# Kernel optimization log

Measured on AMD Instinct MI355X. Metric: run time of the kernel, lower is better.

Reference implementation:

```python
import jax, jax.numpy as jnp
import numpy as np

N, F, D, K, B, L, E, H = 12288, 128, 128, 3, 64, 256, 393216, 8
DT = 2 * D  # token dim
ALPHA = 0.5


def _mlp(h, w1, b1, w2, b2):
    return jax.nn.relu(h @ w1 + b1) @ w2 + b2


def setup_inputs() -> dict:
    key = jax.random.key(0)
    ks = jax.random.split(key, 24)
    s = 0.05
    x = jax.random.normal(ks[0], (N, F), jnp.float32)
    proj_w = jax.random.normal(ks[1], (F, D), jnp.float32) * s
    proj_b = jnp.zeros((D,), jnp.float32)
    adj_rows = jax.random.randint(ks[2], (E,), 0, N, jnp.int32)
    adj_cols = jax.random.randint(ks[3], (E,), 0, N, jnp.int32)
    adj_vals = jax.random.uniform(ks[4], (E,), jnp.float32) / 32.0
    ppr = jax.random.uniform(ks[5], (N, N), jnp.float32) * 0.01
    drnl = jax.random.uniform(ks[6], (B, N), jnp.float32) * 10.0
    src = jax.random.randint(ks[7], (B,), 0, N, jnp.int32)
    dst = jax.random.randint(ks[8], (B,), 0, N, jnp.int32)
    sample_idx = jnp.repeat(jnp.arange(B, dtype=jnp.int32), L)
    node_idx = jax.random.randint(ks[9], (B, L), 0, N, jnp.int32)
    node_idx = node_idx.at[:, 0].set(src).at[:, 1].set(dst).reshape(-1)
    enc_w1 = jax.random.normal(ks[10], (4, 2, D), jnp.float32) * 0.2
    enc_b1 = jnp.zeros((4, D), jnp.float32)
    enc_w2 = jax.random.normal(ks[11], (4, D, D), jnp.float32) * s
    enc_b2 = jnp.zeros((4, D), jnp.float32)
    struct_w1 = jax.random.normal(ks[12], (4 * D, D), jnp.float32) * s
    struct_b1 = jnp.zeros((D,), jnp.float32)
    struct_w2 = jax.random.normal(ks[13], (D, D), jnp.float32) * s
    struct_b2 = jnp.zeros((D,), jnp.float32)
    cls_tok = jax.random.normal(ks[14], (DT,), jnp.float32) * s
    wq = jax.random.normal(ks[15], (DT, DT), jnp.float32) * s
    wk = jax.random.normal(ks[16], (DT, DT), jnp.float32) * s
    wv = jax.random.normal(ks[17], (DT, DT), jnp.float32) * s
    wo = jax.random.normal(ks[18], (DT, DT), jnp.float32) * s
    return dict(x=x, proj_w=proj_w, proj_b=proj_b, adj_vals=adj_vals,
                adj_rows=adj_rows, adj_cols=adj_cols, ppr=ppr, drnl=drnl,
                src=src, dst=dst, sample_idx=sample_idx, node_idx=node_idx,
                enc_w1=enc_w1, enc_b1=enc_b1, enc_w2=enc_w2, enc_b2=enc_b2,
                struct_w1=struct_w1, struct_b1=struct_b1, struct_w2=struct_w2,
                struct_b2=struct_b2, cls_tok=cls_tok, wq=wq, wk=wk, wv=wv, wo=wo)


def reference(x, proj_w, proj_b, adj_vals, adj_rows, adj_cols, ppr, drnl,
              src, dst, sample_idx, node_idx,
              enc_w1, enc_b1, enc_w2, enc_b2,
              struct_w1, struct_b1, struct_w2, struct_b2,
              cls_tok, wq, wk, wv, wo):
    # --- re_features: feature_proj + K sparse matmul hops, APPNP-style mix ---
    feats = x @ proj_w + proj_b                      # [N, D]
    h = feats
    for _ in range(K):
        h = jax.ops.segment_sum(adj_vals[:, None] * h[adj_cols], adj_rows,
                                num_segments=N)      # sparse adj @ h
    re_x = h * (1.0 - ALPHA) + feats * ALPHA         # [N, D]

    # --- cal_heuristic: dense ppr row gather + drnl lookup ---
    n = sample_idx.shape[0]
    ppr_a = ppr[src[sample_idx], node_idx]           # [n]
    ppr_b = ppr[dst[sample_idx], node_idx]
    drnl_v = drnl[sample_idx, node_idx]
    heur = jnp.zeros((n, 4, 2), jnp.float32)
    heur = heur.at[:, 2, 0].set(ppr_a).at[:, 2, 1].set(ppr_b)
    heur = heur.at[:, 3, 0].set(drnl_v).at[:, 3, 1].set(drnl_v)

    # --- tokenizer: 4 heuristic MLPs -> structure MLP, concat node feats ---
    enc = jax.vmap(_mlp)(heur.transpose(1, 0, 2), enc_w1, enc_b1, enc_w2, enc_b2)
    struct_in = enc.transpose(1, 0, 2).reshape(n, 4 * D)   # [n, 4D] (CN,AA,PPR,DRNL)
    struct = _mlp(struct_in, struct_w1, struct_b1, struct_w2, struct_b2)  # [n, D]
    tok = jnp.concatenate([struct, re_x[node_idx]], axis=-1).reshape(B, L, DT)

    # --- GraphTransformer: CLS + multi-head self-attention ---
    cls = jnp.broadcast_to(cls_tok, (B, 1, DT))
    seq = jnp.concatenate([cls, tok], axis=1)        # [B, L+1, DT]
    dh = DT // H
    q = (seq @ wq).reshape(B, L + 1, H, dh)
    k = (seq @ wk).reshape(B, L + 1, H, dh)
    v = (seq @ wv).reshape(B, L + 1, H, dh)
    att = jax.nn.softmax(jnp.einsum('bqhd,bkhd->bhqk', q, k) / jnp.sqrt(jnp.float32(dh)), axis=-1)
    out = jnp.einsum('bhqk,bkhd->bqhd', att, v).reshape(B, L + 1, DT) @ wo
    h_cls, h_a, h_b = out[:, 0], out[:, 1], out[:, 2]
    return jnp.concatenate([h_a, h_b, h_cls], axis=-1)  # [B, 6*dim]
```

## Files before the change

### kernel.cpp

```cpp
#include <hip/hip_runtime.h>
#include <math.h>

#define NN 12288
#define FD 128
#define DD 128
#define EE 393216
#define BB 64
#define LL 256
#define HH 8
#define DTD 256
#define NTOK 16384
#define NSEQ 16448
#define CAP 128

#define SC_B0   0
#define PROJ_B0 1536
#define PREP_B0 1728
#define HEUR_B0 2880
#define SBIAS_B 2944
#define SETUP_GRID 2945

typedef float f32x4 __attribute__((ext_vector_type(4)));
typedef short s16x8 __attribute__((ext_vector_type(8)));

__device__ __forceinline__ float relu_(float x){ return fmaxf(x, 0.0f); }

__device__ __forceinline__ unsigned short f2b(float f){
  unsigned int u = __float_as_uint(f);
  u += 0x7FFFu + ((u >> 16) & 1u);
  return (unsigned short)(u >> 16);
}
__device__ __forceinline__ float b2f(unsigned short h){
  return __uint_as_float(((unsigned int)h) << 16);
}

__device__ __forceinline__ f32x4 MF(s16x8 a, s16x8 b, f32x4 c){
  return __builtin_amdgcn_mfma_f32_16x16x32_bf16(a, b, c, 0, 0, 0);
}

__global__ void __launch_bounds__(256)
k_setup(const float* __restrict__ x, const float* __restrict__ proj_w,
        const float* __restrict__ proj_b, unsigned short* __restrict__ featsb,
        const float* __restrict__ wq, const float* __restrict__ wk,
        const float* __restrict__ wv,
        const float* __restrict__ enc_w2, const float* __restrict__ sw1,
        const float* __restrict__ sw2, const float* __restrict__ cls_tok,
        unsigned short* __restrict__ wqT, unsigned short* __restrict__ wkT,
        unsigned short* __restrict__ wvT,
        unsigned short* __restrict__ w2T2, unsigned short* __restrict__ w2T3,
        unsigned short* __restrict__ sw1aT, unsigned short* __restrict__ sw1bT,
        unsigned short* __restrict__ sw2T, unsigned short* __restrict__ seqb,
        const int* __restrict__ node_idx, const int* __restrict__ srcI,
        const int* __restrict__ dstI, const float* __restrict__ ppr,
        const float* __restrict__ drnl, float* __restrict__ heurA,
        float* __restrict__ heurB, float* __restrict__ heurD,
        const int* __restrict__ adj_rows, const int* __restrict__ adj_cols,
        const float* __restrict__ adj_vals, int* __restrict__ cnt,
        uint2* __restrict__ ccv,
        const float* __restrict__ enc_b1, const float* __restrict__ enc_b2,
        const float* __restrict__ sb1, float* __restrict__ sbias){
  int t = threadIdx.x;
  if(blockIdx.x < PROJ_B0){
    int e = blockIdx.x*256 + t;
    int r = adj_rows[e];
    int p = atomicAdd(&cnt[r], 1);
    ccv[(size_t)r*CAP + p] = make_uint2((unsigned)adj_cols[e], __float_as_uint(adj_vals[e]));
  } else if(blockIdx.x < PREP_B0){
    int bid = blockIdx.x - PROJ_B0;
    int row0 = bid * 64;
    int lane = t & 63, w = t >> 6;
    int lr = lane & 15, lg = lane >> 4;
    f32x4 acc[4][2];
    #pragma unroll
    for(int nt=0;nt<2;++nt){
      int col = w*32 + nt*16 + lr;
      float bv = proj_b[col];
      #pragma unroll
      for(int rt=0;rt<4;++rt)
        #pragma unroll
        for(int i=0;i<4;++i) acc[rt][nt][i]=bv;
    }
    #pragma unroll
    for(int ks=0; ks<4; ++ks){
      int kb = ks*32 + lg*8;
      s16x8 Bf[2];
      #pragma unroll
      for(int nt=0;nt<2;++nt){
        int col = w*32 + nt*16 + lr;
        #pragma unroll
        for(int i=0;i<8;++i) Bf[nt][i] = (short)f2b(proj_w[(kb+i)*DD + col]);
      }
      #pragma unroll
      for(int rt=0;rt<4;++rt){
        int row = row0 + rt*16 + lr;
        const f32x4* xp = (const f32x4*)(x + (size_t)row*FD + kb);
        f32x4 v0 = xp[0], v1 = xp[1];
        s16x8 Af;
        #pragma unroll
        for(int i=0;i<4;++i){ Af[i] = (short)f2b(v0[i]); Af[4+i] = (short)f2b(v1[i]); }
        #pragma unroll
        for(int nt=0;nt<2;++nt) acc[rt][nt] = MF(Af, Bf[nt], acc[rt][nt]);
      }
    }
    #pragma unroll
    for(int rt=0;rt<4;++rt)
      #pragma unroll
      for(int nt=0;nt<2;++nt)
        #pragma unroll
        for(int i=0;i<4;++i){
          int row = row0 + rt*16 + lg*4 + i;
          int col = w*32 + nt*16 + lr;
          featsb[(size_t)row*DD + col] = f2b(acc[rt][nt][i]);
        }
  } else if(blockIdx.x < HEUR_B0){
    int id = (blockIdx.x - PREP_B0)*256 + t;
    if(id < 196608){
      int m = id >> 16, e = id & 65535;
      int n = e & 255, k = e >> 8;
      const float* s = (m==0)? wq : (m==1)? wk : wv;
      unsigned short* d = (m==0)? wqT : (m==1)? wkT : wvT;
      d[n*256 + k] = f2b(s[k*256 + n]);
    } else if(id < 278528){
      int id2 = id - 196608;
      int m = id2 >> 14, e = id2 & 16383;
      int n = e & 127, k = e >> 7;
      const float* s;
      unsigned short* d;
      if(m==0){ s = enc_w2 + 2*16384; d = w2T2; }
      else if(m==1){ s = enc_w2 + 3*16384; d = w2T3; }
      else if(m==2){ s = sw1 + 256*128; d = sw1aT; }
      else if(m==3){ s = sw1 + 384*128; d = sw1bT; }
      else { s = sw2; d = sw2T; }
      d[n*128 + k] = f2b(s[k*128 + n]);
    } else {
      int id3 = id - 278528;
      int b = id3 >> 8, tt = id3 & 255;
      seqb[(size_t)(b*257)*DTD + tt] = f2b(cls_tok[tt]);
    }
  } else if(blockIdx.x < SBIAS_B){
    int tt = (blockIdx.x - HEUR_B0)*256 + t;
    int s = tt >> 8;
    int node = node_idx[tt];
    heurA[tt] = ppr[(size_t)srcI[s]*NN + node];
    heurB[tt] = ppr[(size_t)dstI[s]*NN + node];
    heurD[tt] = drnl[(size_t)s*NN + node];
  } else {
    __shared__ float h0[DD], h1[DD], e0[DD], e1[DD];
    if(t < DD){
      h0[t] = relu_(enc_b1[0*DD+t]);
      h1[t] = relu_(enc_b1[1*DD+t]);
    }
    __syncthreads();
    if(t < DD){
      float a0 = enc_b2[0*DD+t], a1 = enc_b2[1*DD+t];
      for(int d=0; d<DD; ++d){
        a0 += h0[d]*enc_w2[(0*DD+d)*DD + t];
        a1 += h1[d]*enc_w2[(1*DD+d)*DD + t];
      }
      e0[t]=a0; e1[t]=a1;
    }
    __syncthreads();
    if(t < DD){
      float sv = sb1[t];
      for(int d=0; d<DD; ++d)
        sv += e0[d]*sw1[d*DD + t] + e1[d]*sw1[(DD+d)*DD + t];
      sbias[t]=sv;
    }
  }
}

__global__ void __launch_bounds__(256)
k_spmm_w(const unsigned int* __restrict__ hin32, unsigned int* __restrict__ hout32,
         const int* __restrict__ cnt, const uint2* __restrict__ ccv,
         const unsigned int* __restrict__ featsb32, int finalpass){
  int lane = threadIdx.x & 63;
  int r = blockIdx.x*4 + (threadIdx.x>>6);
  int deg = cnt[r];
  const uint2* base = ccv + (size_t)r*CAP;
  float a0=0.f,a1=0.f,b0=0.f,b1=0.f,c0=0.f,c1=0.f,d0=0.f,d1=0.f;
  int p = 0;
  for(; p+4 <= deg; p += 4){
    uint2 q0 = base[p], q1 = base[p+1], q2 = base[p+2], q3 = base[p+3];
    unsigned u0 = hin32[(size_t)q0.x*64 + lane];
    unsigned u1 = hin32[(size_t)q1.x*64 + lane];
    unsigned u2 = hin32[(size_t)q2.x*64 + lane];
    unsigned u3 = hin32[(size_t)q3.x*64 + lane];
    float v0=__uint_as_float(q0.y), v1=__uint_as_float(q1.y);
    float v2=__uint_as_float(q2.y), v3=__uint_as_float(q3.y);
    a0 += v0*b2f((unsigned short)(u0&0xffffu)); a1 += v0*b2f((unsigned short)(u0>>16));
    b0 += v1*b2f((unsigned short)(u1&0xffffu)); b1 += v1*b2f((unsigned short)(u1>>16));
    c0 += v2*b2f((unsigned short)(u2&0xffffu)); c1 += v2*b2f((unsigned short)(u2>>16));
    d0 += v3*b2f((unsigned short)(u3&0xffffu)); d1 += v3*b2f((unsigned short)(u3>>16));
  }
  for(; p < deg; ++p){
    uint2 q0 = base[p];
    unsigned u0 = hin32[(size_t)q0.x*64 + lane];
    float v0 = __uint_as_float(q0.y);
    a0 += v0*b2f((unsigned short)(u0&0xffffu)); a1 += v0*b2f((unsigned short)(u0>>16));
  }
  a0 += b0 + c0 + d0;
  a1 += b1 + c1 + d1;
  if(finalpass){
    unsigned f = featsb32[(size_t)r*64 + lane];
    a0 = 0.5f*a0 + 0.5f*b2f((unsigned short)(f & 0xffffu));
    a1 = 0.5f*a1 + 0.5f*b2f((unsigned short)(f >> 16));
  }
  hout32[(size_t)r*64 + lane] = (unsigned)f2b(a0) | ((unsigned)f2b(a1) << 16);
}

__global__ void __launch_bounds__(256)
k_tok_mfma(const int* __restrict__ node_idx,
           const float* __restrict__ heurA, const float* __restrict__ heurB,
           const float* __restrict__ heurD,
           const float* __restrict__ enc_w1, const float* __restrict__ enc_b1,
           const unsigned short* __restrict__ w2T2, const unsigned short* __restrict__ w2T3,
           const float* __restrict__ enc_b2,
           const unsigned short* __restrict__ sw1aT, const unsigned short* __restrict__ sw1bT,
           const float* __restrict__ sbias,
           const unsigned short* __restrict__ sw2T, const float* __restrict__ sb2,
           const unsigned short* __restrict__ rexb, unsigned short* __restrict__ seqb){
  __shared__ float sA[64], sB[64], sDV[64];
  __shared__ int sNode[64];
  __shared__ __align__(16) unsigned short e2[64][136];
  __shared__ __align__(16) unsigned short e3[64][136];
  __shared__ __align__(16) unsigned short hid[64][136];

  int tid = threadIdx.x;
  int lane = tid & 63;
  int w = tid >> 6;
  int lr = lane & 15;
  int lg = lane >> 4;
  int t0 = blockIdx.x * 64;
  int bs = t0 >> 8;
  int p0 = t0 & 255;
  int seqrow0 = bs*257 + 1 + p0;

  if(tid < 64){
    int tt = t0 + tid;
    sNode[tid] = node_idx[tt];
    sA[tid]  = heurA[tt];
    sB[tid]  = heurB[tt];
    sDV[tid] = heurD[tt];
  }
  __syncthreads();

  {
    f32x4 acc2[4][2], acc3[4][2];
    #pragma unroll
    for(int nt=0;nt<2;++nt){
      int col = w*32 + nt*16 + lr;
      float b2v = enc_b2[2*DD + col];
      float b3v = enc_b2[3*DD + col];
      #pragma unroll
      for(int rt=0;rt<4;++rt)
        #pragma unroll
        for(int i=0;i<4;++i){ acc2[rt][nt][i]=b2v; acc3[rt][nt][i]=b3v; }
    }
    #pragma unroll
    for(int ks=0; ks<4; ++ks){
      int kb = ks*32 + lg*8;
      float w20[8], w21[8], w3s[8], b2c[8], b3c[8];
      #pragma unroll
      for(int i=0;i<8;++i){
        int k = kb + i;
        w20[i] = enc_w1[4*DD + k];
        w21[i] = enc_w1[5*DD + k];
        w3s[i] = enc_w1[6*DD + k] + enc_w1[7*DD + k];
        b2c[i] = enc_b1[2*DD + k];
        b3c[i] = enc_b1[3*DD + k];
      }
      s16x8 B2[2], B3[2];
      #pragma unroll
      for(int nt=0;nt<2;++nt){
        int col = w*32 + nt*16 + lr;
        B2[nt] = *(const s16x8*)(w2T2 + col*DD + kb);
        B3[nt] = *(const s16x8*)(w2T3 + col*DD + kb);
      }
      #pragma unroll
      for(int rt=0;rt<4;++rt){
        int row = rt*16 + lr;
        float a = sA[row], b = sB[row], dv = sDV[row];
        s16x8 A2, A3;
        #pragma unroll
        for(int i=0;i<8;++i){
          A2[i] = (short)f2b(relu_(a*w20[i] + b*w21[i] + b2c[i]));
          A3[i] = (short)f2b(relu_(dv*w3s[i] + b3c[i]));
        }
        #pragma unroll
        for(int nt=0;nt<2;++nt){
          acc2[rt][nt] = MF(A2, B2[nt], acc2[rt][nt]);
          acc3[rt][nt] = MF(A3, B3[nt], acc3[rt][nt]);
        }
      }
    }
    #pragma unroll
    for(int rt=0;rt<4;++rt)
      #pragma unroll
      for(int nt=0;nt<2;++nt)
        #pragma unroll
        for(int i=0;i<4;++i){
          int row = rt*16 + lg*4 + i;
          int col = w*32 + nt*16 + lr;
          e2[row][col] = f2b(acc2[rt][nt][i]);
          e3[row][col] = f2b(acc3[rt][nt][i]);
        }
  }
  __syncthreads();

  {
    f32x4 acc[4][2];
    #pragma unroll
    for(int nt=0;nt<2;++nt){
      int col = w*32 + nt*16 + lr;
      float sv = sbias[col];
      #pragma unroll
      for(int rt=0;rt<4;++rt)
        #pragma unroll
        for(int i=0;i<4;++i) acc[rt][nt][i]=sv;
    }
    #pragma unroll
    for(int ks=0; ks<4; ++ks){
      int kb = ks*32 + lg*8;
      s16x8 Ba[2], Bb[2];
      #pragma unroll
      for(int nt=0;nt<2;++nt){
        int col = w*32 + nt*16 + lr;
        Ba[nt] = *(const s16x8*)(sw1aT + col*DD + kb);
        Bb[nt] = *(const s16x8*)(sw1bT + col*DD + kb);
      }
      #pragma unroll
      for(int rt=0;rt<4;++rt){
        s16x8 A2 = *(const s16x8*)&e2[rt*16+lr][kb];
        s16x8 A3 = *(const s16x8*)&e3[rt*16+lr][kb];
        #pragma unroll
        for(int nt=0;nt<2;++nt){
          acc[rt][nt] = MF(A2, Ba[nt], acc[rt][nt]);
          acc[rt][nt] = MF(A3, Bb[nt], acc[rt][nt]);
        }
      }
    }
    __syncthreads();
    #pragma unroll
    for(int rt=0;rt<4;++rt)
      #pragma unroll
      for(int nt=0;nt<2;++nt)
        #pragma unroll
        for(int i=0;i<4;++i){
          int row = rt*16 + lg*4 + i;
          int col = w*32 + nt*16 + lr;
          hid[row][col] = f2b(relu_(acc[rt][nt][i]));
        }
  }
  __syncthreads();

  {
    f32x4 acc[4][2];
    #pragma unroll
    for(int nt=0;nt<2;++nt){
      int col = w*32 + nt*16 + lr;
      float bv = sb2[col];
      #pragma unroll
      for(int rt=0;rt<4;++rt)
        #pragma unroll
        for(int i=0;i<4;++i) acc[rt][nt][i]=bv;
    }
    #pragma unroll
    for(int ks=0; ks<4; ++ks){
      int kb = ks*32 + lg*8;
      s16x8 Bc[2];
      #pragma unroll
      for(int nt=0;nt<2;++nt){
        int col = w*32 + nt*16 + lr;
        Bc[nt] = *(const s16x8*)(sw2T + col*DD + kb);
      }
      #pragma unroll
      for(int rt=0;rt<4;++rt){
        s16x8 A = *(const s16x8*)&hid[rt*16+lr][kb];
        #pragma unroll
        for(int nt=0;nt<2;++nt) acc[rt][nt] = MF(A, Bc[nt], acc[rt][nt]);
      }
    }
    #pragma unroll
    for(int rt=0;rt<4;++rt)
      #pragma unroll
      for(int nt=0;nt<2;++nt)
        #pragma unroll
        for(int i=0;i<4;++i){
          int row = rt*16 + lg*4 + i;
          int col = w*32 + nt*16 + lr;
          seqb[(size_t)(seqrow0 + row)*DTD + col] = f2b(acc[rt][nt][i]);
        }
  }

  {
    int row = tid >> 2, l4 = tid & 3;
    int c = l4 * 32;
    int node = sNode[row];
    const unsigned short* rp = rexb + (size_t)node*DD + c;
    unsigned short* op = seqb + (size_t)(seqrow0 + row)*DTD + DD + c;
    #pragma unroll
    for(int j=0;j<4;++j)
      *(s16x8*)(op + j*8) = *(const s16x8*)(rp + j*8);
  }
}

__global__ void __launch_bounds__(256)
k_kv_mfma(const unsigned short* __restrict__ seqb,
          const unsigned short* __restrict__ wkT, const unsigned short* __restrict__ wvT,
          const unsigned short* __restrict__ wqT,
          unsigned short* __restrict__ kbuf, unsigned short* __restrict__ vbuf,
          float* __restrict__ qbuf){
  __shared__ __align__(16) unsigned short stile[64][276];
  int tid = threadIdx.x;
  int lane = tid & 63;
  int w = tid >> 6;
  int lr = lane & 15;
  int lg = lane >> 4;

  if(blockIdx.x < 257){
    int row0 = blockIdx.x * 64;
    int col0 = w * 64;
    f32x4 accK[4][4], accV[4][4];
    #pragma unroll
    for(int rt=0;rt<4;++rt)
      #pragma unroll
      for(int nt=0;nt<4;++nt)
        #pragma unroll
        for(int i=0;i<4;++i){ accK[rt][nt][i]=0.f; accV[rt][nt][i]=0.f; }

    #pragma unroll
    for(int ks=0; ks<8; ++ks){
      int kb = ks*32 + lg*8;
      s16x8 A[4], Bk[4], Bv[4];
      #pragma unroll
      for(int rt=0;rt<4;++rt)
        A[rt] = *(const s16x8*)(seqb + (size_t)(row0 + rt*16 + lr)*DTD + kb);
      #pragma unroll
      for(int nt=0;nt<4;++nt){
        int col = col0 + nt*16 + lr;
        Bk[nt] = *(const s16x8*)(wkT + (size_t)col*DTD + kb);
        Bv[nt] = *(const s16x8*)(wvT + (size_t)col*DTD + kb);
      }
      #pragma unroll
      for(int rt=0;rt<4;++rt)
        #pragma unroll
        for(int nt=0;nt<4;++nt){
          accK[rt][nt] = MF(A[rt], Bk[nt], accK[rt][nt]);
          accV[rt][nt] = MF(A[rt], Bv[nt], accV[rt][nt]);
        }
    }

    #pragma unroll
    for(int rt=0;rt<4;++rt)
      #pragma unroll
      for(int nt=0;nt<4;++nt)
        #pragma unroll
        for(int i=0;i<4;++i)
          stile[rt*16 + lg*4 + i][col0 + nt*16 + lr] = f2b(accK[rt][nt][i]);
    __syncthreads();
    {
      int row = tid >> 2, c = (tid & 3)*64;
      #pragma unroll
      for(int j=0;j<8;++j)
        *(s16x8*)(kbuf + (size_t)(row0+row)*DTD + c + j*8) = *(const s16x8*)&stile[row][c + j*8];
    }
    __syncthreads();
    #pragma unroll
    for(int rt=0;rt<4;++rt)
      #pragma unroll
      for(int nt=0;nt<4;++nt)
        #pragma unroll
        for(int i=0;i<4;++i)
          stile[rt*16 + lg*4 + i][col0 + nt*16 + lr] = f2b(accV[rt][nt][i]);
    __syncthreads();
    {
      int row = tid >> 2, c = (tid & 3)*64;
      #pragma unroll
      for(int j=0;j<8;++j)
        *(s16x8*)(vbuf + (size_t)(row0+row)*DTD + c + j*8) = *(const s16x8*)&stile[row][c + j*8];
    }
  } else {
    int qrow0 = (blockIdx.x - 257) * 64;
    int col0 = w * 64;
    int srow[4];
    #pragma unroll
    for(int rt=0;rt<4;++rt){
      int qr = qrow0 + rt*16 + lr;
      int bb = (qr * 21846) >> 16;
      int pp = qr - bb*3;
      srow[rt] = bb*257 + pp;
    }
    f32x4 acc[4][4];
    #pragma unroll
    for(int rt=0;rt<4;++rt)
      #pragma unroll
      for(int nt=0;nt<4;++nt)
        #pragma unroll
        for(int i=0;i<4;++i) acc[rt][nt][i]=0.f;
    #pragma unroll
    for(int ks=0; ks<8; ++ks){
      int kb = ks*32 + lg*8;
      s16x8 A[4], Bq[4];
      #pragma unroll
      for(int rt=0;rt<4;++rt)
        A[rt] = *(const s16x8*)(seqb + (size_t)srow[rt]*DTD + kb);
      #pragma unroll
      for(int nt=0;nt<4;++nt){
        int col = col0 + nt*16 + lr;
        Bq[nt] = *(const s16x8*)(wqT + (size_t)col*DTD + kb);
      }
      #pragma unroll
      for(int rt=0;rt<4;++rt)
        #pragma unroll
        for(int nt=0;nt<4;++nt)
          acc[rt][nt] = MF(A[rt], Bq[nt], acc[rt][nt]);
    }
    #pragma unroll
    for(int rt=0;rt<4;++rt)
      #pragma unroll
      for(int nt=0;nt<4;++nt)
        #pragma unroll
        for(int i=0;i<4;++i){
          int qr = qrow0 + rt*16 + lg*4 + i;
          int col = col0 + nt*16 + lr;
          qbuf[(size_t)qr*DTD + col] = acc[rt][nt][i];
        }
  }
}

__global__ void __launch_bounds__(256)
k_att2(const float* __restrict__ qbuf,
       const unsigned short* __restrict__ kbuf, const unsigned short* __restrict__ vbuf,
       float* __restrict__ att_o){
  __shared__ float q_s[3][32];
  __shared__ float sc[3][257];
  __shared__ float ppv[8][3][32];
  int t = threadIdx.x;
  int b = blockIdx.x >> 3, h = blockIdx.x & 7;

  if(t < 96){
    int qi = t>>5, dd = t&31;
    q_s[qi][dd] = qbuf[(size_t)(b*3+qi)*DTD + h*32 + dd];
  }
  __syncthreads();
  const float scale = 0.17677669529663687f;
  for(int kk=t; kk<257; kk+=256){
    const unsigned short* kr = kbuf + (size_t)(b*257+kk)*DTD + h*32;
    float kv[32];
    #pragma unroll
    for(int j=0;j<4;++j){
      s16x8 u = *(const s16x8*)(kr + j*8);
      #pragma unroll
      for(int m2=0;m2<8;++m2) kv[j*8+m2] = b2f((unsigned short)u[m2]);
    }
    float d0=0.f,d1=0.f,d2=0.f;
    #pragma unroll
    for(int dd=0;dd<32;++dd){
      d0 += q_s[0][dd]*kv[dd]; d1 += q_s[1][dd]*kv[dd]; d2 += q_s[2][dd]*kv[dd];
    }
    sc[0][kk]=d0*scale; sc[1][kk]=d1*scale; sc[2][kk]=d2*scale;
  }
  __syncthreads();
  {
    int wv = t>>6, lane = t&63;
    if(wv < 3){
      int qi = wv;
      float x0=sc[qi][lane], x1=sc[qi][lane+64], x2=sc[qi][lane+128], x3=sc[qi][lane+192];
      float x4 = (lane==0)? sc[qi][256] : -1e30f;
      float m = fmaxf(fmaxf(fmaxf(x0,x1),fmaxf(x2,x3)),x4);
      #pragma unroll
      for(int off=32; off>0; off>>=1) m = fmaxf(m, __shfl_xor(m, off));
      float e0=expf(x0-m), e1=expf(x1-m), e2v=expf(x2-m), e3v=expf(x3-m);
      float e4=(lane==0)? expf(x4-m) : 0.f;
      float s = e0+e1+e2v+e3v+e4;
      #pragma unroll
      for(int off=32; off>0; off>>=1) s += __shfl_xor(s, off);
      float inv = 1.0f/s;
      sc[qi][lane]=e0*inv; sc[qi][lane+64]=e1*inv;
      sc[qi][lane+128]=e2v*inv; sc[qi][lane+192]=e3v*inv;
      if(lane==0) sc[qi][256]=e4*inv;
    }
  }
  __syncthreads();
  {
    int dd = t & 31, g = t >> 5;
    float a0=0.f, a1=0.f, a2=0.f;
    for(int kk=g; kk<257; kk+=8){
      float v = b2f(vbuf[(size_t)(b*257+kk)*DTD + h*32 + dd]);
      a0 += sc[0][kk]*v; a1 += sc[1][kk]*v; a2 += sc[2][kk]*v;
    }
    ppv[g][0][dd]=a0; ppv[g][1][dd]=a1; ppv[g][2][dd]=a2;
  }
  __syncthreads();
  if(t < 96){
    int qi = t>>5, dd = t&31;
    float s = 0.f;
    #pragma unroll
    for(int gg=0; gg<8; ++gg) s += ppv[gg][qi][dd];
    att_o[(size_t)(b*3+qi)*DTD + h*32 + dd] = s;
  }
}

__global__ void k_out(const float* __restrict__ att_o, const float* __restrict__ wo,
                      float* __restrict__ out){
  __shared__ float srow[DTD];
  int t = threadIdx.x;
  int r = blockIdx.x;
  int b = r/3, qi = r - b*3;
  srow[t] = att_o[(size_t)r*DTD + t];
  __syncthreads();
  float acc = 0.f;
  for(int d=0; d<DTD; ++d) acc += srow[d]*wo[d*DTD + t];
  int off = (qi==1)? 0 : ((qi==2)? DTD : 2*DTD);
  out[(size_t)b*768 + off + t] = acc;
}

extern "C" void kernel_launch(void* const* d_in, const int* in_sizes, int n_in,
                              void* d_out, int out_size, void* d_ws, size_t ws_size,
                              hipStream_t stream){
  const float* x        = (const float*)d_in[0];
  const float* proj_w   = (const float*)d_in[1];
  const float* proj_b   = (const float*)d_in[2];
  const float* adj_vals = (const float*)d_in[3];
  const int*   adj_rows = (const int*)d_in[4];
  const int*   adj_cols = (const int*)d_in[5];
  const float* ppr      = (const float*)d_in[6];
  const float* drnl     = (const float*)d_in[7];
  const int*   srcI     = (const int*)d_in[8];
  const int*   dstI     = (const int*)d_in[9];
  const int*   node_idx   = (const int*)d_in[11];
  const float* enc_w1   = (const float*)d_in[12];
  const float* enc_b1   = (const float*)d_in[13];
  const float* enc_w2   = (const float*)d_in[14];
  const float* enc_b2   = (const float*)d_in[15];
  const float* sw1      = (const float*)d_in[16];
  const float* sb1      = (const float*)d_in[17];
  const float* sw2      = (const float*)d_in[18];
  const float* sb2      = (const float*)d_in[19];
  const float* cls_tok  = (const float*)d_in[20];
  const float* wq       = (const float*)d_in[21];
  const float* wk       = (const float*)d_in[22];
  const float* wv       = (const float*)d_in[23];
  const float* wo       = (const float*)d_in[24];
  float* out = (float*)d_out;

  char* p = (char*)d_ws;
  auto alloc = [&](size_t bytes)->void*{ void* r = (void*)p; p += (bytes + 63) & ~(size_t)63; return r; };
  unsigned short* featsb = (unsigned short*)alloc((size_t)NN*DD*2);
  unsigned short* h1b    = (unsigned short*)alloc((size_t)NN*DD*2);
  unsigned short* h2b    = (unsigned short*)alloc((size_t)NN*DD*2);
  unsigned short* rexb   = (unsigned short*)alloc((size_t)NN*DD*2);
  int*   cnt     = (int*)  alloc((size_t)NN*4);
  uint2* ccv     = (uint2*)alloc((size_t)NN*CAP*8);
  float* sbias   = (float*)alloc((size_t)DD*4);
  float* heurA   = (float*)alloc((size_t)NTOK*4);
  float* heurB   = (float*)alloc((size_t)NTOK*4);
  float* heurD   = (float*)alloc((size_t)NTOK*4);
  unsigned short* kbuf = (unsigned short*)alloc((size_t)NSEQ*DTD*2);
  unsigned short* vbuf = (unsigned short*)alloc((size_t)NSEQ*DTD*2);
  float* qbuf    = (float*)alloc((size_t)BB*3*DTD*4);
  float* att_o   = (float*)alloc((size_t)BB*3*DTD*4);
  unsigned short* seqb  = (unsigned short*)alloc((size_t)NSEQ*DTD*2);
  unsigned short* wqT   = (unsigned short*)alloc((size_t)DTD*DTD*2);
  unsigned short* wkT   = (unsigned short*)alloc((size_t)DTD*DTD*2);
  unsigned short* wvT   = (unsigned short*)alloc((size_t)DTD*DTD*2);
  unsigned short* w2T2  = (unsigned short*)alloc((size_t)DD*DD*2);
  unsigned short* w2T3  = (unsigned short*)alloc((size_t)DD*DD*2);
  unsigned short* sw1aT = (unsigned short*)alloc((size_t)DD*DD*2);
  unsigned short* sw1bT = (unsigned short*)alloc((size_t)DD*DD*2);
  unsigned short* sw2T  = (unsigned short*)alloc((size_t)DD*DD*2);

  hipMemsetAsync(cnt, 0, NN*sizeof(int), stream);

  k_setup   <<<SETUP_GRID, 256, 0, stream>>>(x, proj_w, proj_b, featsb,
                                             wq, wk, wv, enc_w2, sw1, sw2, cls_tok,
                                             wqT, wkT, wvT, w2T2, w2T3, sw1aT, sw1bT, sw2T, seqb,
                                             node_idx, srcI, dstI, ppr, drnl,
                                             heurA, heurB, heurD,
                                             adj_rows, adj_cols, adj_vals, cnt, ccv,
                                             enc_b1, enc_b2, sb1, sbias);
  k_spmm_w  <<<NN/4,   256, 0, stream>>>((const unsigned*)featsb, (unsigned*)h1b, cnt, ccv, (const unsigned*)featsb, 0);
  k_spmm_w  <<<NN/4,   256, 0, stream>>>((const unsigned*)h1b, (unsigned*)h2b, cnt, ccv, (const unsigned*)featsb, 0);
  k_spmm_w  <<<NN/4,   256, 0, stream>>>((const unsigned*)h2b, (unsigned*)rexb, cnt, ccv, (const unsigned*)featsb, 1);
  k_tok_mfma<<<NTOK/64,256, 0, stream>>>(node_idx, heurA, heurB, heurD,
                                         enc_w1, enc_b1, w2T2, w2T3, enc_b2,
                                         sw1aT, sw1bT, sbias, sw2T, sb2, rexb, seqb);
  k_kv_mfma <<<260,    256, 0, stream>>>(seqb, wkT, wvT, wqT, kbuf, vbuf, qbuf);
  k_att2    <<<BB*HH,  256, 0, stream>>>(qbuf, kbuf, vbuf, att_o);
  k_out     <<<BB*3,   256, 0, stream>>>(att_o, wo, out);
}
```

Measured before the change: 165.6 us.

## Fuse tokenizer with K/V projection and precompute CLS Q/K/V once

Merges the tokenizer kernel with the K/V/Q projection kernel, so each 64-token tile of the sequence stays in shared memory and goes straight into the K/V MFMA. This drops the global seqb round trip and one kernel launch. The CLS token's Q/K/V, which is the same for every batch, is now computed once in a setup block and read by the attention kernel. In exchange the fused kernel uses more shared memory and registers, and the per-sample Q rows are computed with a scalar loop in the first tile of each sample.

```diff
diff --git a/kernel.cpp b/kernel.cpp
--- a/kernel.cpp
+++ b/kernel.cpp
@@ -10,15 +10,17 @@
 #define HH 8
 #define DTD 256
 #define NTOK 16384
-#define NSEQ 16448
 #define CAP 128
 
-#define SC_B0   0
 #define PROJ_B0 1536
 #define PREP_B0 1728
-#define HEUR_B0 2880
-#define SBIAS_B 2944
-#define SETUP_GRID 2945
+#define HEUR_B0 2816
+#define SBIAS_B 2880
+#define CLS_B   2881
+#define SETUP_GRID 2882
+
+#define SEQ_ST 272
+#define STG_ST 272
 
 typedef float f32x4 __attribute__((ext_vector_type(4)));
 typedef short s16x8 __attribute__((ext_vector_type(8)));
@@ -49,7 +51,7 @@
         unsigned short* __restrict__ wvT,
         unsigned short* __restrict__ w2T2, unsigned short* __restrict__ w2T3,
         unsigned short* __restrict__ sw1aT, unsigned short* __restrict__ sw1bT,
-        unsigned short* __restrict__ sw2T, unsigned short* __restrict__ seqb,
+        unsigned short* __restrict__ sw2T,
         const int* __restrict__ node_idx, const int* __restrict__ srcI,
         const int* __restrict__ dstI, const float* __restrict__ ppr,
         const float* __restrict__ drnl, float* __restrict__ heurA,
@@ -58,7 +60,9 @@
         const float* __restrict__ adj_vals, int* __restrict__ cnt,
         uint2* __restrict__ ccv,
         const float* __restrict__ enc_b1, const float* __restrict__ enc_b2,
-        const float* __restrict__ sb1, float* __restrict__ sbias){
+        const float* __restrict__ sb1, float* __restrict__ sbias,
+        float* __restrict__ qcls, unsigned short* __restrict__ kcls,
+        unsigned short* __restrict__ vcls){
   int t = threadIdx.x;
   if(blockIdx.x < PROJ_B0){
     int e = blockIdx.x*256 + t;
@@ -120,7 +124,7 @@
       const float* s = (m==0)? wq : (m==1)? wk : wv;
       unsigned short* d = (m==0)? wqT : (m==1)? wkT : wvT;
       d[n*256 + k] = f2b(s[k*256 + n]);
-    } else if(id < 278528){
+    } else {
       int id2 = id - 196608;
       int m = id2 >> 14, e = id2 & 16383;
       int n = e & 127, k = e >> 7;
@@ -132,10 +136,6 @@
       else if(m==3){ s = sw1 + 384*128; d = sw1bT; }
       else { s = sw2; d = sw2T; }
       d[n*128 + k] = f2b(s[k*128 + n]);
-    } else {
-      int id3 = id - 278528;
-      int b = id3 >> 8, tt = id3 & 255;
-      seqb[(size_t)(b*257)*DTD + tt] = f2b(cls_tok[tt]);
     }
   } else if(blockIdx.x < SBIAS_B){
     int tt = (blockIdx.x - HEUR_B0)*256 + t;
@@ -144,7 +144,7 @@
     heurA[tt] = ppr[(size_t)srcI[s]*NN + node];
     heurB[tt] = ppr[(size_t)dstI[s]*NN + node];
     heurD[tt] = drnl[(size_t)s*NN + node];
-  } else {
+  } else if(blockIdx.x == SBIAS_B){
     __shared__ float h0[DD], h1[DD], e0[DD], e1[DD];
     if(t < DD){
       h0[t] = relu_(enc_b1[0*DD+t]);
@@ -166,6 +166,20 @@
         sv += e0[d]*sw1[d*DD + t] + e1[d]*sw1[(DD+d)*DD + t];
       sbias[t]=sv;
     }
+  } else {
+    __shared__ float scls[DTD];
+    scls[t] = cls_tok[t];
+    __syncthreads();
+    float aq=0.f, ak=0.f, av=0.f;
+    for(int d=0; d<DTD; ++d){
+      float cv = scls[d];
+      aq += cv*wq[d*DTD + t];
+      ak += cv*wk[d*DTD + t];
+      av += cv*wv[d*DTD + t];
+    }
+    qcls[t] = aq;
+    kcls[t] = f2b(ak);
+    vcls[t] = f2b(av);
   }
 }
 
@@ -209,21 +223,28 @@
 }
 
 __global__ void __launch_bounds__(256)
-k_tok_mfma(const int* __restrict__ node_idx,
-           const float* __restrict__ heurA, const float* __restrict__ heurB,
-           const float* __restrict__ heurD,
-           const float* __restrict__ enc_w1, const float* __restrict__ enc_b1,
-           const unsigned short* __restrict__ w2T2, const unsigned short* __restrict__ w2T3,
-           const float* __restrict__ enc_b2,
-           const unsigned short* __restrict__ sw1aT, const unsigned short* __restrict__ sw1bT,
-           const float* __restrict__ sbias,
-           const unsigned short* __restrict__ sw2T, const float* __restrict__ sb2,
-           const unsigned short* __restrict__ rexb, unsigned short* __restrict__ seqb){
+k_tok_kv(const int* __restrict__ node_idx,
+         const float* __restrict__ heurA, const float* __restrict__ heurB,
+         const float* __restrict__ heurD,
+         const float* __restrict__ enc_w1, const float* __restrict__ enc_b1,
+         const unsigned short* __restrict__ w2T2, const unsigned short* __restrict__ w2T3,
+         const float* __restrict__ enc_b2,
+         const unsigned short* __restrict__ sw1aT, const unsigned short* __restrict__ sw1bT,
+         const float* __restrict__ sbias,
+         const unsigned short* __restrict__ sw2T, const float* __restrict__ sb2,
+         const unsigned short* __restrict__ rexb,
+         const unsigned short* __restrict__ wkT, const unsigned short* __restrict__ wvT,
+         const unsigned short* __restrict__ wqT,
+         unsigned short* __restrict__ kbuf, unsigned short* __restrict__ vbuf,
+         float* __restrict__ qbuf){
   __shared__ float sA[64], sB[64], sDV[64];
   __shared__ int sNode[64];
-  __shared__ __align__(16) unsigned short e2[64][136];
-  __shared__ __align__(16) unsigned short e3[64][136];
-  __shared__ __align__(16) unsigned short hid[64][136];
+  __shared__ __align__(16) unsigned short hid[64*136];
+  __shared__ __align__(16) unsigned short uni[64*STG_ST];
+  unsigned short* pe2 = uni;
+  unsigned short* pe3 = uni + 64*136;
+  unsigned short* seq = uni;
+  unsigned short* stg = uni;
 
   int tid = threadIdx.x;
   int lane = tid & 63;
@@ -233,7 +254,6 @@
   int t0 = blockIdx.x * 64;
   int bs = t0 >> 8;
   int p0 = t0 & 255;
-  int seqrow0 = bs*257 + 1 + p0;
 
   if(tid < 64){
     int tt = t0 + tid;
@@ -301,8 +321,8 @@
         for(int i=0;i<4;++i){
           int row = rt*16 + lg*4 + i;
           int col = w*32 + nt*16 + lr;
-          e2[row][col] = f2b(acc2[rt][nt][i]);
-          e3[row][col] = f2b(acc3[rt][nt][i]);
+          pe2[row*136 + col] = f2b(acc2[rt][nt][i]);
+          pe3[row*136 + col] = f2b(acc3[rt][nt][i]);
         }
   }
   __syncthreads();
@@ -330,8 +350,8 @@
       }
       #pragma unroll
       for(int rt=0;rt<4;++rt){
-        s16x8 A2 = *(const s16x8*)&e2[rt*16+lr][kb];
-        s16x8 A3 = *(const s16x8*)&e3[rt*16+lr][kb];
+        s16x8 A2 = *(const s16x8*)&pe2[(rt*16+lr)*136 + kb];
+        s16x8 A3 = *(const s16x8*)&pe3[(rt*16+lr)*136 + kb];
         #pragma unroll
         for(int nt=0;nt<2;++nt){
           acc[rt][nt] = MF(A2, Ba[nt], acc[rt][nt]);
@@ -348,7 +368,7 @@
         for(int i=0;i<4;++i){
           int row = rt*16 + lg*4 + i;
           int col = w*32 + nt*16 + lr;
-          hid[row][col] = f2b(relu_(acc[rt][nt][i]));
+          hid[row*136 + col] = f2b(relu_(acc[rt][nt][i]));
         }
   }
   __syncthreads();
@@ -375,7 +395,7 @@
       }
       #pragma unroll
       for(int rt=0;rt<4;++rt){
-        s16x8 A = *(const s16x8*)&hid[rt*16+lr][kb];
+        s16x8 A = *(const s16x8*)&hid[(rt*16+lr)*136 + kb];
         #pragma unroll
         for(int nt=0;nt<2;++nt) acc[rt][nt] = MF(A, Bc[nt], acc[rt][nt]);
       }
@@ -388,53 +408,34 @@
         for(int i=0;i<4;++i){
           int row = rt*16 + lg*4 + i;
           int col = w*32 + nt*16 + lr;
-          seqb[(size_t)(seqrow0 + row)*DTD + col] = f2b(acc[rt][nt][i]);
-        }
-  }
-
-  {
+          seq[row*SEQ_ST + col] = f2b(acc[rt][nt][i]);
+        }
     int row = tid >> 2, l4 = tid & 3;
     int c = l4 * 32;
     int node = sNode[row];
     const unsigned short* rp = rexb + (size_t)node*DD + c;
-    unsigned short* op = seqb + (size_t)(seqrow0 + row)*DTD + DD + c;
     #pragma unroll
     for(int j=0;j<4;++j)
-      *(s16x8*)(op + j*8) = *(const s16x8*)(rp + j*8);
-  }
-}
-
-__global__ void __launch_bounds__(256)
-k_kv_mfma(const unsigned short* __restrict__ seqb,
-          const unsigned short* __restrict__ wkT, const unsigned short* __restrict__ wvT,
-          const unsigned short* __restrict__ wqT,
-          unsigned short* __restrict__ kbuf, unsigned short* __restrict__ vbuf,
-          float* __restrict__ qbuf){
-  __shared__ __align__(16) unsigned short stile[64][276];
-  int tid = threadIdx.x;
-  int lane = tid & 63;
-  int w = tid >> 6;
-  int lr = lane & 15;
-  int lg = lane >> 4;
-
-  if(blockIdx.x < 257){
-    int row0 = blockIdx.x * 64;
+      *(s16x8*)(seq + row*SEQ_ST + DD + c + j*8) = *(const s16x8*)(rp + j*8);
+  }
+  __syncthreads();
+
+  f32x4 accK[4][4], accV[4][4];
+  {
+    #pragma unroll
+    for(int rt=0;rt<4;++rt)
+      #pragma unroll
+      for(int nt=0;nt<4;++nt)
+        #pragma unroll
+        for(int i=0;i<4;++i){ accK[rt][nt][i]=0.f; accV[rt][nt][i]=0.f; }
     int col0 = w * 64;
-    f32x4 accK[4][4], accV[4][4];
-    #pragma unroll
-    for(int rt=0;rt<4;++rt)
-      #pragma unroll
-      for(int nt=0;nt<4;++nt)
-        #pragma unroll
-        for(int i=0;i<4;++i){ accK[rt][nt][i]=0.f; accV[rt][nt][i]=0.f; }
-
     #pragma unroll
     for(int ks=0; ks<8; ++ks){
       int kb = ks*32 + lg*8;
       s16x8 A[4], Bk[4], Bv[4];
       #pragma unroll
       for(int rt=0;rt<4;++rt)
-        A[rt] = *(const s16x8*)(seqb + (size_t)(row0 + rt*16 + lr)*DTD + kb);
+        A[rt] = *(const s16x8*)&seq[(rt*16+lr)*SEQ_ST + kb];
       #pragma unroll
       for(int nt=0;nt<4;++nt){
         int col = col0 + nt*16 + lr;
@@ -449,87 +450,63 @@
           accV[rt][nt] = MF(A[rt], Bv[nt], accV[rt][nt]);
         }
     }
-
+  }
+  if(p0 == 0){
+    #pragma unroll
+    for(int qi=0; qi<2; ++qi){
+      int col = w*64 + lane;
+      float acc = 0.f;
+      for(int d=0; d<DTD; d+=8){
+        s16x8 wv8 = *(const s16x8*)(wqT + (size_t)col*DTD + d);
+        #pragma unroll
+        for(int j=0;j<8;++j)
+          acc += b2f(seq[qi*SEQ_ST + d + j]) * b2f((unsigned short)wv8[j]);
+      }
+      qbuf[(size_t)(bs*2+qi)*DTD + col] = acc;
+    }
+  }
+  __syncthreads();
+
+  {
+    int col0 = w * 64;
     #pragma unroll
     for(int rt=0;rt<4;++rt)
       #pragma unroll
       for(int nt=0;nt<4;++nt)
         #pragma unroll
         for(int i=0;i<4;++i)
-          stile[rt*16 + lg*4 + i][col0 + nt*16 + lr] = f2b(accK[rt][nt][i]);
-    __syncthreads();
-    {
-      int row = tid >> 2, c = (tid & 3)*64;
-      #pragma unroll
-      for(int j=0;j<8;++j)
-        *(s16x8*)(kbuf + (size_t)(row0+row)*DTD + c + j*8) = *(const s16x8*)&stile[row][c + j*8];
-    }
-    __syncthreads();
+          stg[(rt*16 + lg*4 + i)*STG_ST + col0 + nt*16 + lr] = f2b(accK[rt][nt][i]);
+  }
+  __syncthreads();
+  {
+    int row = tid >> 2, c = (tid & 3)*64;
+    #pragma unroll
+    for(int j=0;j<8;++j)
+      *(s16x8*)(kbuf + (size_t)(t0+row)*DTD + c + j*8) = *(const s16x8*)&stg[row*STG_ST + c + j*8];
+  }
+  __syncthreads();
+  {
+    int col0 = w * 64;
     #pragma unroll
     for(int rt=0;rt<4;++rt)
       #pragma unroll
       for(int nt=0;nt<4;++nt)
         #pragma unroll
         for(int i=0;i<4;++i)
-          stile[rt*16 + lg*4 + i][col0 + nt*16 + lr] = f2b(accV[rt][nt][i]);
-    __syncthreads();
-    {
-      int row = tid >> 2, c = (tid & 3)*64;
-      #pragma unroll
-      for(int j=0;j<8;++j)
-        *(s16x8*)(vbuf + (size_t)(row0+row)*DTD + c + j*8) = *(const s16x8*)&stile[row][c + j*8];
-    }
-  } else {
-    int qrow0 = (blockIdx.x - 257) * 64;
-    int col0 = w * 64;
-    int srow[4];
-    #pragma unroll
-    for(int rt=0;rt<4;++rt){
-      int qr = qrow0 + rt*16 + lr;
-      int bb = (qr * 21846) >> 16;
-      int pp = qr - bb*3;
-      srow[rt] = bb*257 + pp;
-    }
-    f32x4 acc[4][4];
-    #pragma unroll
-    for(int rt=0;rt<4;++rt)
-      #pragma unroll
-      for(int nt=0;nt<4;++nt)
-        #pragma unroll
-        for(int i=0;i<4;++i) acc[rt][nt][i]=0.f;
-    #pragma unroll
-    for(int ks=0; ks<8; ++ks){
-      int kb = ks*32 + lg*8;
-      s16x8 A[4], Bq[4];
-      #pragma unroll
-      for(int rt=0;rt<4;++rt)
-        A[rt] = *(const s16x8*)(seqb + (size_t)srow[rt]*DTD + kb);
-      #pragma unroll
-      for(int nt=0;nt<4;++nt){
-        int col = col0 + nt*16 + lr;
-        Bq[nt] = *(const s16x8*)(wqT + (size_t)col*DTD + kb);
-      }
-      #pragma unroll
-      for(int rt=0;rt<4;++rt)
-        #pragma unroll
-        for(int nt=0;nt<4;++nt)
-          acc[rt][nt] = MF(A[rt], Bq[nt], acc[rt][nt]);
-    }
-    #pragma unroll
-    for(int rt=0;rt<4;++rt)
-      #pragma unroll
-      for(int nt=0;nt<4;++nt)
-        #pragma unroll
-        for(int i=0;i<4;++i){
-          int qr = qrow0 + rt*16 + lg*4 + i;
-          int col = col0 + nt*16 + lr;
-          qbuf[(size_t)qr*DTD + col] = acc[rt][nt][i];
-        }
+          stg[(rt*16 + lg*4 + i)*STG_ST + col0 + nt*16 + lr] = f2b(accV[rt][nt][i]);
+  }
+  __syncthreads();
+  {
+    int row = tid >> 2, c = (tid & 3)*64;
+    #pragma unroll
+    for(int j=0;j<8;++j)
+      *(s16x8*)(vbuf + (size_t)(t0+row)*DTD + c + j*8) = *(const s16x8*)&stg[row*STG_ST + c + j*8];
   }
 }
 
 __global__ void __launch_bounds__(256)
-k_att2(const float* __restrict__ qbuf,
+k_att2(const float* __restrict__ qcls, const float* __restrict__ qbuf,
+       const unsigned short* __restrict__ kcls, const unsigned short* __restrict__ vcls,
        const unsigned short* __restrict__ kbuf, const unsigned short* __restrict__ vbuf,
        float* __restrict__ att_o){
   __shared__ float q_s[3][32];
@@ -540,12 +517,14 @@
 
   if(t < 96){
     int qi = t>>5, dd = t&31;
-    q_s[qi][dd] = qbuf[(size_t)(b*3+qi)*DTD + h*32 + dd];
+    q_s[qi][dd] = (qi==0) ? qcls[h*32 + dd]
+                          : qbuf[(size_t)(b*2+qi-1)*DTD + h*32 + dd];
   }
   __syncthreads();
   const float scale = 0.17677669529663687f;
   for(int kk=t; kk<257; kk+=256){
-    const unsigned short* kr = kbuf + (size_t)(b*257+kk)*DTD + h*32;
+    const unsigned short* kr = (kk==0) ? (kcls + h*32)
+                                       : (kbuf + (size_t)(b*256+kk-1)*DTD + h*32);
     float kv[32];
     #pragma unroll
     for(int j=0;j<4;++j){
@@ -586,7 +565,9 @@
     int dd = t & 31, g = t >> 5;
     float a0=0.f, a1=0.f, a2=0.f;
     for(int kk=g; kk<257; kk+=8){
-      float v = b2f(vbuf[(size_t)(b*257+kk)*DTD + h*32 + dd]);
+      const unsigned short* vr = (kk==0) ? (vcls + h*32)
+                                         : (vbuf + (size_t)(b*256+kk-1)*DTD + h*32);
+      float v = b2f(vr[dd]);
       a0 += sc[0][kk]*v; a1 += sc[1][kk]*v; a2 += sc[2][kk]*v;
     }
     ppv[g][0][dd]=a0; ppv[g][1][dd]=a1; ppv[g][2][dd]=a2;
@@ -656,11 +637,13 @@
   float* heurA   = (float*)alloc((size_t)NTOK*4);
   float* heurB   = (float*)alloc((size_t)NTOK*4);
   float* heurD   = (float*)alloc((size_t)NTOK*4);
-  unsigned short* kbuf = (unsigned short*)alloc((size_t)NSEQ*DTD*2);
-  unsigned short* vbuf = (unsigned short*)alloc((size_t)NSEQ*DTD*2);
-  float* qbuf    = (float*)alloc((size_t)BB*3*DTD*4);
+  unsigned short* kbuf = (unsigned short*)alloc((size_t)NTOK*DTD*2);
+  unsigned short* vbuf = (unsigned short*)alloc((size_t)NTOK*DTD*2);
+  float* qbuf    = (float*)alloc((size_t)BB*2*DTD*4);
+  float* qcls    = (float*)alloc((size_t)DTD*4);
+  unsigned short* kcls = (unsigned short*)alloc((size_t)DTD*2);
+  unsigned short* vcls = (unsigned short*)alloc((size_t)DTD*2);
   float* att_o   = (float*)alloc((size_t)BB*3*DTD*4);
-  unsigned short* seqb  = (unsigned short*)alloc((size_t)NSEQ*DTD*2);
   unsigned short* wqT   = (unsigned short*)alloc((size_t)DTD*DTD*2);
   unsigned short* wkT   = (unsigned short*)alloc((size_t)DTD*DTD*2);
   unsigned short* wvT   = (unsigned short*)alloc((size_t)DTD*DTD*2);
@@ -672,20 +655,21 @@
 
   hipMemsetAsync(cnt, 0, NN*sizeof(int), stream);
 
-  k_setup   <<<SETUP_GRID, 256, 0, stream>>>(x, proj_w, proj_b, featsb,
-                                             wq, wk, wv, enc_w2, sw1, sw2, cls_tok,
-                                             wqT, wkT, wvT, w2T2, w2T3, sw1aT, sw1bT, sw2T, seqb,
-                                             node_idx, srcI, dstI, ppr, drnl,
-                                             heurA, heurB, heurD,
-                                             adj_rows, adj_cols, adj_vals, cnt, ccv,
-                                             enc_b1, enc_b2, sb1, sbias);
-  k_spmm_w  <<<NN/4,   256, 0, stream>>>((const unsigned*)featsb, (unsigned*)h1b, cnt, ccv, (const unsigned*)featsb, 0);
-  k_spmm_w  <<<NN/4,   256, 0, stream>>>((const unsigned*)h1b, (unsigned*)h2b, cnt, ccv, (const unsigned*)featsb, 0);
-  k_spmm_w  <<<NN/4,   256, 0, stream>>>((const unsigned*)h2b, (unsigned*)rexb, cnt, ccv, (const unsigned*)featsb, 1);
-  k_tok_mfma<<<NTOK/64,256, 0, stream>>>(node_idx, heurA, heurB, heurD,
-                                         enc_w1, enc_b1, w2T2, w2T3, enc_b2,
-                                         sw1aT, sw1bT, sbias, sw2T, sb2, rexb, seqb);
-  k_kv_mfma <<<260,    256, 0, stream>>>(seqb, wkT, wvT, wqT, kbuf, vbuf, qbuf);
-  k_att2    <<<BB*HH,  256, 0, stream>>>(qbuf, kbuf, vbuf, att_o);
-  k_out     <<<BB*3,   256, 0, stream>>>(att_o, wo, out);
-}
+  k_setup  <<<SETUP_GRID, 256, 0, stream>>>(x, proj_w, proj_b, featsb,
+                                            wq, wk, wv, enc_w2, sw1, sw2, cls_tok,
+                                            wqT, wkT, wvT, w2T2, w2T3, sw1aT, sw1bT, sw2T,
+                                            node_idx, srcI, dstI, ppr, drnl,
+                                            heurA, heurB, heurD,
+                                            adj_rows, adj_cols, adj_vals, cnt, ccv,
+                                            enc_b1, enc_b2, sb1, sbias,
+                                            qcls, kcls, vcls);
+  k_spmm_w <<<NN/4,   256, 0, stream>>>((const unsigned*)featsb, (unsigned*)h1b, cnt, ccv, (const unsigned*)featsb, 0);
+  k_spmm_w <<<NN/4,   256, 0, stream>>>((const unsigned*)h1b, (unsigned*)h2b, cnt, ccv, (const unsigned*)featsb, 0);
+  k_spmm_w <<<NN/4,   256, 0, stream>>>((const unsigned*)h2b, (unsigned*)rexb, cnt, ccv, (const unsigned*)featsb, 1);
+  k_tok_kv <<<NTOK/64,256, 0, stream>>>(node_idx, heurA, heurB, heurD,
+                                        enc_w1, enc_b1, w2T2, w2T3, enc_b2,
+                                        sw1aT, sw1bT, sbias, sw2T, sb2, rexb,
+                                        wkT, wvT, wqT, kbuf, vbuf, qbuf);
+  k_att2   <<<BB*HH,  256, 0, stream>>>(qcls, qbuf, kcls, vcls, kbuf, vbuf, att_o);
+  k_out    <<<BB*3,   256, 0, stream>>>(att_o, wo, out);
+}
```

After: 155.7 us. 5.9% less time.
